# Kernel tuning notes

Measured on AMD Instinct MI355X. Metric: run time of the kernel, lower is better.

## Reference

```python
import jax, jax.numpy as jnp
import numpy as np

N_HEADS = 2
N_POINTS = 3
BN_EPS = 1e-5


def make_pe(C, D):
    # PositionalEncoding buffer, sliced to depth D: shape (D, C)
    pos = np.arange(D, dtype=np.float32)[:, None]
    div = np.exp(np.arange(0, C, 2, dtype=np.float32) * (-np.log(10000.0) / C))
    pe = np.zeros((D, C), dtype=np.float32)
    pe[:, 0::2] = np.sin(pos * div)
    pe[:, 1::2] = np.cos(pos * div)
    return jnp.asarray(pe)


def setup_inputs() -> dict:
    key = jax.random.key(0)
    b, c, zs, h, w = 2, 256, 32, 48, 48
    hp = N_HEADS * N_POINTS
    ks = jax.random.split(key, 8)
    features = jax.random.normal(ks[0], (b, c, zs, h, w), dtype=jnp.float32)
    # 1x1 Conv3d weights (out_ch, in_ch), no bias
    q_w = jax.random.normal(ks[1], (c, c), dtype=jnp.float32) * 0.05
    v_w = jax.random.normal(ks[2], (c, c), dtype=jnp.float32) * 0.05
    o_w = jax.random.normal(ks[3], (c, c), dtype=jnp.float32) * 0.05
    # sampling_offsets Linear: module inits weight=0, bias=[-1,-2,-3,1,2,3];
    # we add small random weight so sampling is input-dependent (non-degenerate)
    offs_w = jax.random.normal(ks[4], (hp, c), dtype=jnp.float32) * 0.02
    direction = np.array([[-1.0, -2.0, -3.0], [1.0, 2.0, 3.0]], dtype=np.float32)
    offs_b = jnp.asarray(direction.reshape(-1))
    attn_w = jax.random.normal(ks[5], (hp, c), dtype=jnp.float32) * 0.02
    attn_b = jax.random.normal(ks[6], (hp,), dtype=jnp.float32) * 0.1
    gamma = jnp.ones((c,), dtype=jnp.float32)
    beta = jnp.zeros((c,), dtype=jnp.float32)
    return {"features": features, "q_w": q_w, "v_w": v_w, "o_w": o_w,
            "offs_w": offs_w, "offs_b": offs_b, "attn_w": attn_w,
            "attn_b": attn_b, "gamma": gamma, "beta": beta}


def reference(features, q_w, v_w, o_w, offs_w, offs_b, attn_w, attn_b, gamma, beta):
    b, c, zs, h, w = features.shape
    pe = make_pe(c, zs)  # (zs, c)
    x = features + pe.T[None, :, :, None, None]  # (b,c,zs,h,w)
    # 1x1 conv3d == per-voxel channel GEMM
    q = jnp.einsum('oc,bcdhw->bodhw', q_w, x)
    v = jnp.einsum('oc,bcdhw->bodhw', v_w, x)
    # AdaptiveMaxPool1d(1) over h*w -> global spatial max; (b,zs,c)
    qp = jnp.transpose(q.max(axis=(3, 4)), (0, 2, 1))
    off = jnp.clip(qp @ offs_w.T + offs_b, 0.0, zs - 1)      # (b,zs,hp)
    attn = jax.nn.softmax(qp @ attn_w.T + attn_b, axis=-1)    # (b,zs,hp)
    lo = jnp.floor(off)
    hi = jnp.ceil(off)
    frac = off - lo
    # gather index depends only on (b,zs,hp), not (c,h,w): fold the
    # interp-weighted gather into a per-batch (zs_out, zs_in) mixing matrix.
    w_lo = attn * (1.0 - frac)
    w_hi = attn * frac
    oh_lo = jax.nn.one_hot(lo.astype(jnp.int32), zs, dtype=features.dtype)
    oh_hi = jax.nn.one_hot(hi.astype(jnp.int32), zs, dtype=features.dtype)
    M = (oh_lo * w_lo[..., None] + oh_hi * w_hi[..., None]).sum(axis=2)  # (b,zs,zs)
    samp = jnp.einsum('bzy,bcyhw->bczhw', M, v)  # (b,c,zs,h,w)
    out = jnp.einsum('oc,bcdhw->bodhw', o_w, samp)
    # BatchNorm3d, training-mode batch statistics (biased var), eps=1e-5
    mean = out.mean(axis=(0, 2, 3, 4))
    var = out.var(axis=(0, 2, 3, 4))
    normed = (out - mean[None, :, None, None, None]) * jax.lax.rsqrt(var + BN_EPS)[None, :, None, None, None]
    normed = normed * gamma[None, :, None, None, None] + beta[None, :, None, None, None]
    return normed + features
```

## Files before the change

### kernel.cpp

```cpp
#include <hip/hip_runtime.h>


#define B_   2
#define C_   256
#define Z_   32
#define HW_  2304
#define NSP  73728
#define NBN  147456.0f

typedef unsigned short u16;
typedef unsigned int   u32;
typedef __attribute__((ext_vector_type(8))) short bf16x8;
typedef __attribute__((ext_vector_type(4))) float f32x4;

__device__ int   g_isf32;
__device__ int   g_use_mfma;
__device__ float g_pe[Z_ * C_];
__device__ __align__(16) float g_wt[C_ * 512];
__device__ __align__(16) u16   g_afrag[32 * 8 * 2 * 64 * 8];
__device__ int   g_qmax[B_ * Z_ * C_];
__device__ __align__(16) float g_Mt[B_ * Z_ * Z_];
__device__ float g_bn_sum[C_];
__device__ float g_bn_ssq[C_];
__device__ float g_u[(size_t)B_ * C_ * NSP];

__device__ __forceinline__ u16 f2bf(float f) {
  u32 x = __float_as_uint(f);
  x = x + 0x7fffu + ((x >> 16) & 1u);
  return (u16)(x >> 16);
}
__device__ __forceinline__ float bf2f(u16 h) {
  return __uint_as_float(((u32)h) << 16);
}
__device__ __forceinline__ float ldx(const void* p, size_t i, int f32) {
  if (f32) return ((const float*)p)[i];
  return __uint_as_float(((u32)((const u16*)p)[i]) << 16);
}
__device__ __forceinline__ void stx(void* p, size_t i, int f32, float v) {
  if (f32) ((float*)p)[i] = v;
  else     ((u16*)p)[i] = f2bf(v);
}
__device__ __forceinline__ int f2key(float f) {
  int b = __float_as_int(f);
  return b >= 0 ? b : (b ^ 0x7fffffff);
}
__device__ __forceinline__ float key2f(int k) {
  int b = k >= 0 ? k : (k ^ 0x7fffffff);
  return __int_as_float(b);
}
__device__ __forceinline__ float sane(float v) {
  u32 a = __float_as_uint(v) & 0x7fffffffu;
  return (a >= 0x7f800000u) ? 0.f : v;
}
__device__ __forceinline__ float wredmax(float m) {
  m = fmaxf(m, __shfl_xor(m, 1));  m = fmaxf(m, __shfl_xor(m, 2));
  m = fmaxf(m, __shfl_xor(m, 4));  m = fmaxf(m, __shfl_xor(m, 8));
  m = fmaxf(m, __shfl_xor(m, 16)); m = fmaxf(m, __shfl_xor(m, 32));
  return m;
}
__device__ __forceinline__ float wredsum(float s) {
  s += __shfl_xor(s, 1);  s += __shfl_xor(s, 2);  s += __shfl_xor(s, 4);
  s += __shfl_xor(s, 8);  s += __shfl_xor(s, 16); s += __shfl_xor(s, 32);
  return s;
}


__device__ __forceinline__ void stage_x(const void* __restrict__ f, int f32,
                                        int b, int z, int ncol0, u16* xs) {
  const int tid = threadIdx.x;
  const int w = tid >> 6, l = tid & 63;
  const int n0 = (l & 15) * 4;
  const int g = l >> 4;
  for (int r = 0; r < 16; ++r) {
    const int k = r * 16 + w * 4 + g;
    const float pv = g_pe[z * C_ + k];
    const size_t fe = (size_t)(b * C_ + k) * NSP + ncol0 + n0;
    float x0, x1, x2, x3;
    if (f32) {
      const float4 v = *(const float4*)((const float*)f + fe);
      x0 = v.x; x1 = v.y; x2 = v.z; x3 = v.w;
    } else {
      x0 = ldx(f, fe + 0, 0); x1 = ldx(f, fe + 1, 0);
      x2 = ldx(f, fe + 2, 0); x3 = ldx(f, fe + 3, 0);
    }
    x0 += pv; x1 += pv; x2 += pv; x3 += pv;
#pragma unroll
    for (int e = 0; e < 4; ++e) {
      const float xv = (e == 0) ? x0 : (e == 1) ? x1 : (e == 2) ? x2 : x3;
      const int n = n0 + e;
      u16 hi = f2bf(xv);
      u16 lo = f2bf(xv - bf2f(hi));
      u32 byte = (u32)n * 512u + (u32)k * 2u;
      byte ^= (u32)(n & 15) << 4;
      xs[byte >> 1] = hi;
      xs[(byte >> 1) + 16384] = lo;
    }
  }
}

__device__ __forceinline__ bf16x8 read_bfrag(const u16* xs, int j, int kk,
                                             int plane, int lane) {
  const int n = j * 16 + (lane & 15);
  u32 byte = (u32)plane * 32768u + (u32)n * 512u + (u32)kk * 64u + (u32)(lane >> 4) * 16u;
  byte ^= (u32)(n & 15) << 4;
  return *(const bf16x8*)(const void*)((const char*)xs + byte);
}

__device__ __forceinline__ bf16x8 load_afrag(int rs, int kk, int plane, int lane) {
  const size_t off = ((((size_t)(rs * 8 + kk) * 2 + plane) * 64 + lane) * 8);
  return *(const bf16x8*)(const void*)(g_afrag + off);
}

__device__ __forceinline__ f32x4 mfma3(bf16x8 ah, bf16x8 al,
                                       bf16x8 bh, bf16x8 bl, f32x4 acc) {
  acc = __builtin_amdgcn_mfma_f32_16x16x32_bf16(ah, bh, acc, 0, 0, 0);
  acc = __builtin_amdgcn_mfma_f32_16x16x32_bf16(ah, bl, acc, 0, 0, 0);
  acc = __builtin_amdgcn_mfma_f32_16x16x32_bf16(al, bh, acc, 0, 0, 0);
  return acc;
}

__global__ void k00_detect(const void* f) {
  const int t = threadIdx.x;
  u32 w = ((const u32*)f)[(size_t)t * 9973u];
  u32 e = (w >> 7) & 0xFFu;
  int in = (e >= 90u && e <= 140u) ? 1 : 0;
  for (int o = 1; o < 64; o <<= 1) in += __shfl_xor(in, o);
  if (t == 0) g_isf32 = (in < 40) ? 1 : 0;
}

__device__ __forceinline__ void pack_afrag(int row, int k, float val) {
  const int rs = row >> 4, kk = k >> 5, i = k & 7, g = (k >> 3) & 3;
  const int l = (row & 15) | (g << 4);
  u16 hi = f2bf(val);
  u16 lo = f2bf(val - bf2f(hi));
  const size_t u = (((size_t)(rs * 8 + kk) * 2) * 64 + l) * 8 + i;
  g_afrag[u] = hi;
  g_afrag[u + 512] = lo;
}

__global__ __launch_bounds__(256) void k0_setup(const void* o_w, const void* v_w,
                                                const void* q_w) {
  const int f32 = g_isf32;
  const int blk = blockIdx.x, t = threadIdx.x;
  if (blk < 256) {
    float acc = 0.f;
    for (int c = 0; c < 256; ++c)
      acc += ldx(o_w, (size_t)blk * 256 + c, f32) * ldx(v_w, (size_t)c * 256 + t, f32);
    g_wt[(size_t)t * 512 + blk] = acc;
    const float qv = ldx(q_w, (size_t)blk * 256 + t, f32);
    g_wt[(size_t)t * 512 + 256 + blk] = qv;
    pack_afrag(blk, t, acc);
    pack_afrag(256 + blk, t, qv);
  } else {
    const int ch = t;
    const float divf = expf(-(float)(ch >> 1) * (9.210340371976184f / 128.0f));
    for (int z = 0; z < Z_; ++z) {
      float arg = (float)z * divf;
      g_pe[z * 256 + ch] = (ch & 1) ? cosf(arg) : sinf(arg);
    }
    const int init_key = f2key(-1e30f);
    for (int k = t; k < B_ * Z_ * 256; k += 256) g_qmax[k] = init_key;
    g_bn_sum[t] = 0.f;
    g_bn_ssq[t] = 0.f;
  }
}

__global__ __launch_bounds__(256) void kP_probe(const void* __restrict__ f) {
  __shared__ u16 xs[32768];
  const int f32 = g_isf32;
  stage_x(f, f32, 0, 0, 0, xs);
  __syncthreads();
  if (threadIdx.x < 64) {
    const int lane = threadIdx.x;
    f32x4 acc = {0.f, 0.f, 0.f, 0.f};
    for (int kk = 0; kk < 8; ++kk) {
      bf16x8 bh = read_bfrag(xs, 0, kk, 0, lane);
      bf16x8 bl = read_bfrag(xs, 0, kk, 1, lane);
      bf16x8 ah = load_afrag(0, kk, 0, lane);
      bf16x8 al = load_afrag(0, kk, 1, lane);
      acc = mfma3(ah, al, bh, bl, acc);
    }
    int ok = 1;
    const int col = lane & 15;
#pragma unroll
    for (int reg = 0; reg < 4; ++reg) {
      const int row = (lane >> 4) * 4 + reg;
      float ref = 0.f;
      for (int k = 0; k < 256; ++k)
        ref = fmaf(g_wt[(size_t)k * 512 + row],
                   ldx(f, (size_t)k * NSP + col, f32) + g_pe[k], ref);
      ok &= (fabsf(acc[reg] - ref) <= 0.02f + 0.01f * fabsf(ref)) ? 1 : 0;
    }
    ok = __all(ok);
    if (lane == 0) g_use_mfma = ok;
  }
}

__global__ __launch_bounds__(256) void kA_mfma(const void* __restrict__ f) {
  if (!g_use_mfma) return;
  __shared__ u16 xs[32768];
  const int f32 = g_isf32;
  const int id = blockIdx.x;
  const int b = id / 1152;
  const int r2 = id % 1152;
  const int z = r2 / 36;
  const int m = r2 % 36;
  const int ncol0 = z * HW_ + m * 64;
  const int tid = threadIdx.x, w = tid >> 6, lane = tid & 63;

  stage_x(f, f32, b, z, ncol0, xs);
  __syncthreads();

  f32x4 acc[8][4];
  const f32x4 z4 = {0.f, 0.f, 0.f, 0.f};
#pragma unroll
  for (int r = 0; r < 8; ++r)
#pragma unroll
    for (int j = 0; j < 4; ++j) acc[r][j] = z4;

  for (int kk = 0; kk < 8; ++kk) {
    bf16x8 bh[4], bl[4];
#pragma unroll
    for (int j = 0; j < 4; ++j) {
      bh[j] = read_bfrag(xs, j, kk, 0, lane);
      bl[j] = read_bfrag(xs, j, kk, 1, lane);
    }
#pragma unroll
    for (int rsl = 0; rsl < 8; ++rsl) {
      const int rs = w * 8 + rsl;
      bf16x8 ah = load_afrag(rs, kk, 0, lane);
      bf16x8 al = load_afrag(rs, kk, 1, lane);
#pragma unroll
      for (int j = 0; j < 4; ++j)
        acc[rsl][j] = mfma3(ah, al, bh[j], bl[j], acc[rsl][j]);
    }
  }

  if (w < 2) {
#pragma unroll
    for (int rsl = 0; rsl < 8; ++rsl)
#pragma unroll
      for (int j = 0; j < 4; ++j)
#pragma unroll
        for (int reg = 0; reg < 4; ++reg) {
          const int row = (w * 8 + rsl) * 16 + (lane >> 4) * 4 + reg;
          g_u[(size_t)(b * C_ + row) * NSP + ncol0 + j * 16 + (lane & 15)] =
              acc[rsl][j][reg];
        }
  } else {
    const int rbase = (b * Z_ + z) * C_;
#pragma unroll
    for (int rsl = 0; rsl < 8; ++rsl)
#pragma unroll
      for (int reg = 0; reg < 4; ++reg) {
        float v = fmaxf(fmaxf(acc[rsl][0][reg], acc[rsl][1][reg]),
                        fmaxf(acc[rsl][2][reg], acc[rsl][3][reg]));
        v = fmaxf(v, __shfl_xor(v, 1));
        v = fmaxf(v, __shfl_xor(v, 2));
        v = fmaxf(v, __shfl_xor(v, 4));
        v = fmaxf(v, __shfl_xor(v, 8));
        if ((lane & 15) == 0)
          atomicMax(&g_qmax[rbase + ((w - 2) * 8 + rsl) * 16 + (lane >> 4) * 4 + reg],
                    f2key(v));
      }
  }
}

template<int F32>
__global__ __launch_bounds__(256) void kA_gemm(const void* __restrict__ f) {
  if (g_isf32 != F32) return;
  if (g_use_mfma) return;
  const int bid = blockIdx.x;
  const int k  = bid & 7;
  const int jj = bid >> 3;
  const int T  = k + 8 * (jj >> 3);
  const int g  = jj & 7;
  const int b  = T / 288;
  const int tz = T % 288;
  const int z  = tz / 9;
  const int hc = tz % 9;
  const int t  = threadIdx.x;
  const int n_in_z = hc * 256 + t;
  const size_t fbase = (size_t)(b * C_) * NSP + (size_t)z * HW_ + n_in_z;

  float acc[64];
#pragma unroll
  for (int i = 0; i < 64; ++i) acc[i] = 0.f;

  const float* __restrict__ wtb = g_wt + g * 64;
  const float* __restrict__ pez = g_pe + z * C_;
  for (int c = 0; c < C_; ++c) {
    float fv = ldx(f, fbase + (size_t)c * NSP, F32) + pez[c];
    const float4* __restrict__ w4 = (const float4*)(wtb + (size_t)c * 512);
#pragma unroll
    for (int q = 0; q < 16; ++q) {
      float4 wv = w4[q];
      acc[4*q+0] = fmaf(wv.x, fv, acc[4*q+0]);
      acc[4*q+1] = fmaf(wv.y, fv, acc[4*q+1]);
      acc[4*q+2] = fmaf(wv.z, fv, acc[4*q+2]);
      acc[4*q+3] = fmaf(wv.w, fv, acc[4*q+3]);
    }
  }

  if (g < 4) {
    const size_t obase = (size_t)(b * C_ + g * 64) * NSP + (size_t)z * HW_ + n_in_z;
#pragma unroll
    for (int i = 0; i < 64; ++i)
      g_u[obase + (size_t)i * NSP] = acc[i];
  } else {
    const int rbase = (b * Z_ + z) * C_ + (g - 4) * 64;
#pragma unroll
    for (int i = 0; i < 64; ++i) {
      float mres = wredmax(acc[i]);
      if ((t & 63) == 0) atomicMax(&g_qmax[rbase + i], f2key(mres));
    }
  }
}

__global__ __launch_bounds__(64) void k2_mbuild(
    const void* offs_w, const void* offs_b,
    const void* attn_w, const void* attn_b) {
  const int f32 = g_isf32;
  const int bz = blockIdx.x;
  const int lane = threadIdx.x;
  float qp[4];
#pragma unroll
  for (int i = 0; i < 4; ++i)
    qp[i] = key2f(g_qmax[bz * 256 + lane * 4 + i]);

  float res[12];
  for (int p = 0; p < 12; ++p) {
    const void* wm = (p < 6) ? offs_w : attn_w;
    const size_t row = (size_t)(p < 6 ? p : p - 6) * 256;
    float s = 0.f;
#pragma unroll
    for (int i = 0; i < 4; ++i) s += qp[i] * ldx(wm, row + lane * 4 + i, f32);
    res[p] = sane(wredsum(s));
  }

  __shared__ float sm[Z_];
  if (lane < Z_) sm[lane] = 0.f;
  __syncthreads();
  if (lane == 0) {
    float att[6], mx = -1e30f;
#pragma unroll
    for (int p = 0; p < 6; ++p) {
      att[p] = sane(res[6 + p] + ldx(attn_b, p, f32));
      mx = fmaxf(mx, att[p]);
    }
    float den = 0.f;
#pragma unroll
    for (int p = 0; p < 6; ++p) { att[p] = expf(att[p] - mx); den += att[p]; }
    float inv = 1.f / den;
#pragma unroll
    for (int p = 0; p < 6; ++p) {
      float a = att[p] * inv;
      float off = sane(res[p] + ldx(offs_b, p, f32));
      off = fminf(fmaxf(off, 0.f), 31.f);
      float lo = floorf(off), hi = ceilf(off), fr = off - lo;
      int il = min(max((int)lo, 0), 31);
      int ih = min(max((int)hi, 0), 31);
      sm[il] += a * (1.f - fr);
      sm[ih] += a * fr;
    }
  }
  __syncthreads();
  if (lane < Z_) g_Mt[((bz >> 5) * Z_ + lane) * Z_ + (bz & 31)] = sm[lane];
}

__global__ __launch_bounds__(256) void kB_mix(void* outp) {
  const int f32 = g_isf32;
  const int id = blockIdx.x;
  const int b = id / 2304;
  const int rem = id % 2304;
  const int o = rem / 9;
  const int hc = rem % 9;
  const int hw = hc * 256 + threadIdx.x;
  const size_t base = (size_t)(b * C_ + o) * NSP + hw;

  float a[Z_];
#pragma unroll
  for (int zo = 0; zo < Z_; ++zo) a[zo] = 0.f;

  for (int y = 0; y < Z_; ++y) {
    float uv = g_u[base + (size_t)y * HW_];
    const float4* __restrict__ m4 = (const float4*)(g_Mt + (size_t)(b * Z_ + y) * Z_);
#pragma unroll
    for (int q = 0; q < 8; ++q) {
      float4 mv = m4[q];
      a[4*q+0] = fmaf(mv.x, uv, a[4*q+0]);
      a[4*q+1] = fmaf(mv.y, uv, a[4*q+1]);
      a[4*q+2] = fmaf(mv.z, uv, a[4*q+2]);
      a[4*q+3] = fmaf(mv.w, uv, a[4*q+3]);
    }
  }

  float s = 0.f, ss = 0.f;
#pragma unroll
  for (int zo = 0; zo < Z_; ++zo) {
    float v = sane(a[zo]);
    stx(outp, base + (size_t)zo * HW_, f32, v);
    s += v;  ss += v * v;
  }
  s = wredsum(s);
  ss = wredsum(ss);
  if ((threadIdx.x & 63) == 0) {
    atomicAdd(&g_bn_sum[o], s);
    atomicAdd(&g_bn_ssq[o], ss);
  }
}

__global__ __launch_bounds__(256) void k5_final(
    const void* f, void* outp, const void* gamma, const void* beta) {
  const int f32 = g_isf32;
  const size_t e4 = ((size_t)blockIdx.x * 256 + threadIdx.x) * 4;
  const int o = (int)((e4 / NSP) & 255);
  const float mean = g_bn_sum[o] * (1.f / NBN);
  const float var = fmaxf(g_bn_ssq[o] * (1.f / NBN) - mean * mean, 0.f);
  const float rstd = rsqrtf(var + 1e-5f);
  const float sc = ldx(gamma, o, f32) * rstd;
  const float sh = ldx(beta, o, f32) - mean * sc;
  if (f32) {
    float4 ov = *(float4*)((float*)outp + e4);
    const float4 fv = *(const float4*)((const float*)f + e4);
    ov.x = sane(ov.x * sc + sh + fv.x);
    ov.y = sane(ov.y * sc + sh + fv.y);
    ov.z = sane(ov.z * sc + sh + fv.z);
    ov.w = sane(ov.w * sc + sh + fv.w);
    *(float4*)((float*)outp + e4) = ov;
  } else {
#pragma unroll
    for (int i = 0; i < 4; ++i) {
      float v = sane(ldx(outp, e4 + i, 0) * sc + sh + ldx(f, e4 + i, 0));
      stx(outp, e4 + i, 0, v);
    }
  }
}

extern "C" void kernel_launch(void* const* d_in, const int* in_sizes, int n_in,
                              void* d_out, int out_size, void* d_ws, size_t ws_size,
                              hipStream_t stream)
{
  (void)in_sizes; (void)n_in; (void)out_size; (void)d_ws; (void)ws_size;
  const void* f      = d_in[0];
  const void* q_w    = d_in[1];
  const void* v_w    = d_in[2];
  const void* o_w    = d_in[3];
  const void* offs_w = d_in[4];
  const void* offs_b = d_in[5];
  const void* attn_w = d_in[6];
  const void* attn_b = d_in[7];
  const void* gamma  = d_in[8];
  const void* beta   = d_in[9];

  k00_detect<<<1, 64, 0, stream>>>(f);
  k0_setup<<<257, 256, 0, stream>>>(o_w, v_w, q_w);
  kP_probe<<<1, 256, 0, stream>>>(f);
  kA_mfma<<<2304, 256, 0, stream>>>(f);
  kA_gemm<1><<<4608, 256, 0, stream>>>(f);
  kA_gemm<0><<<4608, 256, 0, stream>>>(f);
  k2_mbuild<<<64, 64, 0, stream>>>(offs_w, offs_b, attn_w, attn_b);
  kB_mix<<<4608, 256, 0, stream>>>(d_out);
  k5_final<<<36864, 256, 0, stream>>>(f, d_out, gamma, beta);
}
```

Baseline: 794.8 us.

## Drop low-order bf16 split of activations and relayout LDS tile into fragment order

The activation operand of the split-bf16 GEMM is no longer decomposed into hi and lo parts, so each tile now uses two MFMAs instead of three and the LDS tile is half its former size. The LDS layout is rearranged so each lane's B fragment is one contiguous 16-byte read with no XOR swizzle, and staging now loads four channel rows per column instead of a float4 along columns. This is meant to cut matrix-core work, LDS traffic and shared-memory footprint. The cost is lower precision in the Q/V projection and less coalesced global loads during staging.

```diff
diff --git a/kernel.cpp b/kernel.cpp
--- a/kernel.cpp
+++ b/kernel.cpp
@@ -69,54 +69,47 @@
                                         int b, int z, int ncol0, u16* xs) {
   const int tid = threadIdx.x;
   const int w = tid >> 6, l = tid & 63;
-  const int n0 = (l & 15) * 4;
-  const int g = l >> 4;
+  const int m  = l & 15;
+  const int g4 = l >> 4;
+  const size_t fcol = (size_t)ncol0 + (w * 16 + m);
+#pragma unroll 4
   for (int r = 0; r < 16; ++r) {
-    const int k = r * 16 + w * 4 + g;
-    const float pv = g_pe[z * C_ + k];
-    const size_t fe = (size_t)(b * C_ + k) * NSP + ncol0 + n0;
+    const int k0 = r * 16 + g4 * 4;
+    const float4 pv = *(const float4*)(g_pe + z * C_ + k0);
+    const size_t fe = (size_t)(b * C_ + k0) * NSP + fcol;
     float x0, x1, x2, x3;
     if (f32) {
-      const float4 v = *(const float4*)((const float*)f + fe);
-      x0 = v.x; x1 = v.y; x2 = v.z; x3 = v.w;
+      const float* ff = (const float*)f;
+      x0 = ff[fe];
+      x1 = ff[fe + (size_t)NSP];
+      x2 = ff[fe + 2 * (size_t)NSP];
+      x3 = ff[fe + 3 * (size_t)NSP];
     } else {
-      x0 = ldx(f, fe + 0, 0); x1 = ldx(f, fe + 1, 0);
-      x2 = ldx(f, fe + 2, 0); x3 = ldx(f, fe + 3, 0);
-    }
-    x0 += pv; x1 += pv; x2 += pv; x3 += pv;
-#pragma unroll
-    for (int e = 0; e < 4; ++e) {
-      const float xv = (e == 0) ? x0 : (e == 1) ? x1 : (e == 2) ? x2 : x3;
-      const int n = n0 + e;
-      u16 hi = f2bf(xv);
-      u16 lo = f2bf(xv - bf2f(hi));
-      u32 byte = (u32)n * 512u + (u32)k * 2u;
-      byte ^= (u32)(n & 15) << 4;
-      xs[byte >> 1] = hi;
-      xs[(byte >> 1) + 16384] = lo;
-    }
-  }
-}
-
-__device__ __forceinline__ bf16x8 read_bfrag(const u16* xs, int j, int kk,
-                                             int plane, int lane) {
-  const int n = j * 16 + (lane & 15);
-  u32 byte = (u32)plane * 32768u + (u32)n * 512u + (u32)kk * 64u + (u32)(lane >> 4) * 16u;
-  byte ^= (u32)(n & 15) << 4;
-  return *(const bf16x8*)(const void*)((const char*)xs + byte);
+      x0 = ldx(f, fe, 0);
+      x1 = ldx(f, fe + (size_t)NSP, 0);
+      x2 = ldx(f, fe + 2 * (size_t)NSP, 0);
+      x3 = ldx(f, fe + 3 * (size_t)NSP, 0);
+    }
+    ushort4 hv;
+    hv.x = f2bf(x0 + pv.x);
+    hv.y = f2bf(x1 + pv.y);
+    hv.z = f2bf(x2 + pv.z);
+    hv.w = f2bf(x3 + pv.w);
+    const u32 byte = (u32)(w * 8 + (r >> 1)) * 1024u
+                   + (u32)(((((r & 1) << 1) | (g4 >> 1)) << 4) | m) * 16u
+                   + (u32)(g4 & 1) * 8u;
+    *(ushort4*)((char*)xs + byte) = hv;
+  }
+}
+
+__device__ __forceinline__ bf16x8 read_bfrag(const u16* xs, int j, int kk, int lane) {
+  return *(const bf16x8*)(const void*)((const char*)xs +
+         ((u32)(j * 8 + kk) * 1024u + (u32)lane * 16u));
 }
 
 __device__ __forceinline__ bf16x8 load_afrag(int rs, int kk, int plane, int lane) {
   const size_t off = ((((size_t)(rs * 8 + kk) * 2 + plane) * 64 + lane) * 8);
   return *(const bf16x8*)(const void*)(g_afrag + off);
-}
-
-__device__ __forceinline__ f32x4 mfma3(bf16x8 ah, bf16x8 al,
-                                       bf16x8 bh, bf16x8 bl, f32x4 acc) {
-  acc = __builtin_amdgcn_mfma_f32_16x16x32_bf16(ah, bh, acc, 0, 0, 0);
-  acc = __builtin_amdgcn_mfma_f32_16x16x32_bf16(ah, bl, acc, 0, 0, 0);
-  acc = __builtin_amdgcn_mfma_f32_16x16x32_bf16(al, bh, acc, 0, 0, 0);
-  return acc;
 }
 
 __global__ void k00_detect(const void* f) {
@@ -166,7 +159,7 @@
 }
 
 __global__ __launch_bounds__(256) void kP_probe(const void* __restrict__ f) {
-  __shared__ u16 xs[32768];
+  __shared__ u16 xs[16384];
   const int f32 = g_isf32;
   stage_x(f, f32, 0, 0, 0, xs);
   __syncthreads();
@@ -174,21 +167,29 @@
     const int lane = threadIdx.x;
     f32x4 acc = {0.f, 0.f, 0.f, 0.f};
     for (int kk = 0; kk < 8; ++kk) {
-      bf16x8 bh = read_bfrag(xs, 0, kk, 0, lane);
-      bf16x8 bl = read_bfrag(xs, 0, kk, 1, lane);
+      bf16x8 bh = read_bfrag(xs, 0, kk, lane);
       bf16x8 ah = load_afrag(0, kk, 0, lane);
       bf16x8 al = load_afrag(0, kk, 1, lane);
-      acc = mfma3(ah, al, bh, bl, acc);
+      acc = __builtin_amdgcn_mfma_f32_16x16x32_bf16(ah, bh, acc, 0, 0, 0);
+      acc = __builtin_amdgcn_mfma_f32_16x16x32_bf16(al, bh, acc, 0, 0, 0);
     }
     int ok = 1;
     const int col = lane & 15;
 #pragma unroll
     for (int reg = 0; reg < 4; ++reg) {
       const int row = (lane >> 4) * 4 + reg;
-      float ref = 0.f;
-      for (int k = 0; k < 256; ++k)
-        ref = fmaf(g_wt[(size_t)k * 512 + row],
-                   ldx(f, (size_t)k * NSP + col, f32) + g_pe[k], ref);
+      float r0 = 0.f, r1 = 0.f, r2 = 0.f, r3 = 0.f;
+      for (int k = 0; k < 256; k += 4) {
+        r0 = fmaf(g_wt[(size_t)(k+0) * 512 + row],
+                  ldx(f, (size_t)(k+0) * NSP + col, f32) + g_pe[k+0], r0);
+        r1 = fmaf(g_wt[(size_t)(k+1) * 512 + row],
+                  ldx(f, (size_t)(k+1) * NSP + col, f32) + g_pe[k+1], r1);
+        r2 = fmaf(g_wt[(size_t)(k+2) * 512 + row],
+                  ldx(f, (size_t)(k+2) * NSP + col, f32) + g_pe[k+2], r2);
+        r3 = fmaf(g_wt[(size_t)(k+3) * 512 + row],
+                  ldx(f, (size_t)(k+3) * NSP + col, f32) + g_pe[k+3], r3);
+      }
+      float ref = (r0 + r1) + (r2 + r3);
       ok &= (fabsf(acc[reg] - ref) <= 0.02f + 0.01f * fabsf(ref)) ? 1 : 0;
     }
     ok = __all(ok);
@@ -198,7 +199,7 @@
 
 __global__ __launch_bounds__(256) void kA_mfma(const void* __restrict__ f) {
   if (!g_use_mfma) return;
-  __shared__ u16 xs[32768];
+  __shared__ u16 xs[16384];
   const int f32 = g_isf32;
   const int id = blockIdx.x;
   const int b = id / 1152;
@@ -218,21 +219,21 @@
 #pragma unroll
     for (int j = 0; j < 4; ++j) acc[r][j] = z4;
 
+#pragma unroll 2
   for (int kk = 0; kk < 8; ++kk) {
-    bf16x8 bh[4], bl[4];
-#pragma unroll
-    for (int j = 0; j < 4; ++j) {
-      bh[j] = read_bfrag(xs, j, kk, 0, lane);
-      bl[j] = read_bfrag(xs, j, kk, 1, lane);
-    }
+    bf16x8 bh[4];
+#pragma unroll
+    for (int j = 0; j < 4; ++j) bh[j] = read_bfrag(xs, j, kk, lane);
 #pragma unroll
     for (int rsl = 0; rsl < 8; ++rsl) {
       const int rs = w * 8 + rsl;
       bf16x8 ah = load_afrag(rs, kk, 0, lane);
       bf16x8 al = load_afrag(rs, kk, 1, lane);
 #pragma unroll
-      for (int j = 0; j < 4; ++j)
-        acc[rsl][j] = mfma3(ah, al, bh[j], bl[j], acc[rsl][j]);
+      for (int j = 0; j < 4; ++j) {
+        acc[rsl][j] = __builtin_amdgcn_mfma_f32_16x16x32_bf16(ah, bh[j], acc[rsl][j], 0, 0, 0);
+        acc[rsl][j] = __builtin_amdgcn_mfma_f32_16x16x32_bf16(al, bh[j], acc[rsl][j], 0, 0, 0);
+      }
     }
   }
 
```

Result: slower. 961.0 us (+20.9%).
